# Kernel optimization log

Hardware: AMD Instinct MI355X
Metric: run time of the kernel (lower is better)

## Reference

```python
import jax, jax.numpy as jnp
import numpy as np

# Int8 fixed-point (power-of-two scale) quant params, mirroring Brevitas
# Int8ActPerTensorFixedPoint / Uint8ActPerTensorFixedPoint with fixed learned scales.
QMAX, QMIN, UQMAX = 127.0, -128.0, 255.0
IO_SCALE = 2.0 ** -4    # io_quant (int8) range ~ [-8, 7.94]
ACC_SCALE = 2.0 ** -3   # gate_acc_quant (int8) range ~ [-16, 15.875]
SIG_SCALE = 2.0 ** -8   # sigmoid_quant (uint8) range [0, ~0.996]
TANH_SCALE = 2.0 ** -7  # tanh_quant (int8) range ~ [-1, 0.992]


def ste_round(x):
    return x + jax.lax.stop_gradient(jnp.round(x) - x)


def qd(x, scale, qmin, qmax):
    # quantize-dequantize with straight-through rounding
    return scale * jnp.clip(ste_round(x / scale), qmin, qmax)


def quant_weight(w):
    # Int8WeightPerTensorFixedPoint: power-of-two per-tensor scale from max-abs stats
    maxabs = jax.lax.stop_gradient(jnp.max(jnp.abs(w)))
    scale = jax.lax.stop_gradient(2.0 ** jnp.ceil(jnp.log2(maxabs / QMAX)))
    return qd(w, scale, QMIN, QMAX)


def setup_inputs() -> dict:
    key = jax.random.key(0)
    ks = jax.random.split(key, 8)
    B, S, V, E, H, O = 64, 512, 32000, 512, 512, 2
    return {
        "text": jax.random.randint(ks[0], (B, S), 0, V, dtype=jnp.int32),
        "text_lengths": jax.random.randint(ks[1], (B,), 1, S, dtype=jnp.int32),
        "emb_w": jax.random.normal(ks[2], (V, E), jnp.float32) * 0.05,
        "w_ih": jax.random.normal(ks[3], (4 * H, E), jnp.float32) * 0.05,
        "w_hh": jax.random.normal(ks[4], (4 * H, H), jnp.float32) * 0.05,
        "b_ih": jax.random.normal(ks[5], (4 * H,), jnp.float32) * 0.05,
        "b_hh": jax.random.normal(ks[6], (4 * H,), jnp.float32) * 0.05,
        "fc_w": jax.random.normal(ks[7], (O, H), jnp.float32) * 0.05,
    }


def reference(text, text_lengths, emb_w, w_ih, w_hh, b_ih, b_hh, fc_w):
    B = text.shape[0]
    H = w_hh.shape[1]

    # quantized embedding lookup + io quant on LSTM input
    x = quant_weight(emb_w)[text]               # [B,S,E]
    x = qd(x, IO_SCALE, QMIN, QMAX)

    wih_q = quant_weight(w_ih)
    whh_q = quant_weight(w_hh)

    # precompute input contribution to gates: [B,S,4H]
    xg = jnp.einsum("bse,ge->bsg", x, wih_q) + b_ih + b_hh

    def step(carry, xg_t):
        h, c = carry
        gates = qd(xg_t + h @ whh_q.T, ACC_SCALE, QMIN, QMAX)  # gate_acc quant
        i, f, g, o = jnp.split(gates, 4, axis=-1)
        i = qd(jax.nn.sigmoid(i), SIG_SCALE, 0.0, UQMAX)
        f = qd(jax.nn.sigmoid(f), SIG_SCALE, 0.0, UQMAX)
        o = qd(jax.nn.sigmoid(o), SIG_SCALE, 0.0, UQMAX)
        g = qd(jnp.tanh(g), TANH_SCALE, QMIN, QMAX)
        c = f * c + i * g
        h = qd(o * qd(jnp.tanh(c), TANH_SCALE, QMIN, QMAX), IO_SCALE, QMIN, QMAX)
        return (h, c), h

    h0 = jnp.zeros((B, H), x.dtype)
    (hT, cT), _ = jax.lax.scan(step, (h0, h0), jnp.swapaxes(xg, 0, 1))

    hidden_state = hT[None]                     # [1,B,H] like torch LSTM
    return hidden_state @ quant_weight(fc_w).T  # [1,B,O]
```

## Files before the change

### kernel.cpp

```cpp
#include <hip/hip_runtime.h>
#include <math.h>

#define S_LEN  512
#define BATCH  64
#define E_DIM  512
#define H_DIM  512
#define G4     2048
#define VOCAB  32000
#define NWG    16

typedef int v4i __attribute__((ext_vector_type(4)));
typedef unsigned long long u64;

#define O_BAR   0
#define O_MAX   256
#define O_H8    512
#define O_FC8   131584
#define O_WIH8  132608
#define O_WHH8  (O_WIH8 + 1048576)
#define O_X8    (O_WHH8 + 1048576)

__device__ __forceinline__ float clampf(float x, float lo, float hi) {
    return fminf(fmaxf(x, lo), hi);
}

__device__ __forceinline__ int scale_exp(float maxabs) {
    double t = (double)maxabs / 127.0;
    int e; double f = frexp(t, &e);
    return (f == 0.5) ? (e - 1) : e;
}

__device__ __forceinline__ float xla_tanhf(float x) {
    if (fabsf(x) < 0.0004f) return x;
    float xc = fminf(fmaxf(x, -7.90531110763549805f), 7.90531110763549805f);
    float x2 = __fmul_rn(xc, xc);
    float p = fmaf(x2, -2.76076847742355e-16f, 2.00018790482477e-13f);
    p = fmaf(x2, p, -8.60467152213735e-11f);
    p = fmaf(x2, p, 5.12229709037114e-08f);
    p = fmaf(x2, p, 1.48572235717979e-05f);
    p = fmaf(x2, p, 6.37261928875436e-04f);
    p = fmaf(x2, p, 4.89352455891786e-03f);
    p = __fmul_rn(xc, p);
    float q = fmaf(x2, 1.19825839466702e-06f, 1.18534705686654e-04f);
    q = fmaf(x2, q, 2.26843463243900e-03f);
    q = fmaf(x2, q, 4.89352518554385e-03f);
    return __fdiv_rn(p, q);
}

__global__ void k_maxabs(const float* __restrict__ x, int n, unsigned* __restrict__ out) {
    unsigned m = 0;
    for (int i = blockIdx.x * blockDim.x + threadIdx.x; i < n; i += gridDim.x * blockDim.x)
        m = max(m, __float_as_uint(fabsf(x[i])));
    #pragma unroll
    for (int o = 32; o > 0; o >>= 1) {
        unsigned other = (unsigned)__shfl_down((int)m, o, 64);
        m = max(m, other);
    }
    __shared__ unsigned sm[4];
    if ((threadIdx.x & 63) == 0) sm[threadIdx.x >> 6] = m;
    __syncthreads();
    if (threadIdx.x == 0) {
        unsigned r = sm[0];
        for (int w = 1; w < (int)(blockDim.x >> 6); w++) r = max(r, sm[w]);
        atomicMax(out, r);
    }
}

__global__ void k_quantw(const float* __restrict__ w, int n, const unsigned* __restrict__ mx,
                         signed char* __restrict__ q) {
    float inv = ldexpf(1.0f, -scale_exp(__uint_as_float(*mx)));
    for (int i = blockIdx.x * blockDim.x + threadIdx.x; i < n; i += gridDim.x * blockDim.x) {
        float v = clampf(rintf(w[i] * inv), -128.0f, 127.0f);
        q[i] = (signed char)(int)v;
    }
}

__global__ void k_embed(const float* __restrict__ emb, const int* __restrict__ text,
                        const unsigned* __restrict__ mx, signed char* __restrict__ x8) {
    int row = blockIdx.x;
    int b = row >> 9, s = row & 511;
    int tok = text[row];
    int ke = scale_exp(__uint_as_float(*mx));
    float inv = ldexpf(1.0f, -ke);
    float sc2 = ldexpf(1.0f, ke + 4);
    const float4* src = (const float4*)(emb + (size_t)tok * E_DIM);
    char4* dst = (char4*)(x8 + (size_t)(s * BATCH + b) * E_DIM);
    float4 v = src[threadIdx.x];
    char4 c;
    float q;
    q = clampf(rintf(v.x * inv), -128.f, 127.f); c.x = (signed char)(int)clampf(rintf(q * sc2), -128.f, 127.f);
    q = clampf(rintf(v.y * inv), -128.f, 127.f); c.y = (signed char)(int)clampf(rintf(q * sc2), -128.f, 127.f);
    q = clampf(rintf(v.z * inv), -128.f, 127.f); c.z = (signed char)(int)clampf(rintf(q * sc2), -128.f, 127.f);
    q = clampf(rintf(v.w * inv), -128.f, 127.f); c.w = (signed char)(int)clampf(rintf(q * sc2), -128.f, 127.f);
    dst[threadIdx.x] = c;
}

#define MKFRAG(a, b) ((v4i){(a)[0], (a)[1], (b)[0], (b)[1]})

__global__ __launch_bounds__(256, 1) void k_lstm(
    const signed char* __restrict__ wih8, const signed char* __restrict__ whh8,
    const signed char* __restrict__ x8, const float* __restrict__ b_ih,
    const float* __restrict__ b_hh, const unsigned* __restrict__ mx,
    signed char* __restrict__ h8) {
    __shared__ __attribute__((aligned(16))) signed char wih_lds[128 * 528];
    __shared__ __attribute__((aligned(16))) signed char hstage[BATCH * 32];
    __shared__ float lut_sig[256];
    __shared__ float lut_tnh[256];

    const int g = blockIdx.x;
    const int tid = threadIdx.x;
    const int wv = tid >> 6, lane = tid & 63, l15 = lane & 15, qd4 = lane >> 4;
    const float sih = ldexpf(1.0f, scale_exp(__uint_as_float(mx[1])) - 4);
    const float shh = ldexpf(1.0f, scale_exp(__uint_as_float(mx[2])) - 4);

    if (tid < 256) {
        float v = (float)(tid - 128) * 0.125f;
        float sg = __fadd_rn(0.5f, __fmul_rn(0.5f, xla_tanhf(__fmul_rn(0.5f, v))));
        float sc = clampf(rintf(__fmul_rn(sg, 256.0f)), 0.0f, 255.0f);
        lut_sig[tid] = sc * 0.00390625f;
        float th = xla_tanhf(v);
        float tc = clampf(rintf(__fmul_rn(th, 128.0f)), -128.0f, 127.0f);
        lut_tnh[tid] = tc * 0.0078125f;
    }

    for (int it = 0; it < 16; it++) {
        int idx = it * 256 + tid;
        int r = idx >> 5, cc = (idx & 31) * 16;
        int grow = (r >> 5) * 512 + g * 32 + (r & 31);
        *(v4i*)(wih_lds + r * 528 + cc) = *(const v4i*)(wih8 + (size_t)grow * 512 + cc);
    }

    v4i whf[8][8];
    #pragma unroll
    for (int nt = 0; nt < 8; nt++) {
        int nl = nt * 16 + l15;
        size_t grow = (size_t)((nl >> 5) * 512 + g * 32 + (nl & 31)) * 512;
        #pragma unroll
        for (int k = 0; k < 8; k++)
            whf[nt][k] = *(const v4i*)(whh8 + grow + k * 64 + qd4 * 16);
    }
    __syncthreads();

    float bi[8], bh[8];
    #pragma unroll
    for (int nt = 0; nt < 8; nt++) {
        int nl = nt * 16 + l15;
        int col = (nl >> 5) * 512 + g * 32 + (nl & 31);
        bi[nt] = b_ih[col];
        bh[nt] = b_hh[col];
    }

    float cst[2][4];
    #pragma unroll
    for (int jh = 0; jh < 2; jh++)
        #pragma unroll
        for (int r = 0; r < 4; r++) cst[jh][r] = 0.0f;

    v4i xacc[8];
    {
        v4i xfr[8];
        const signed char* xrow = x8 + (size_t)(wv * 16 + l15) * 512 + qd4 * 16;
        #pragma unroll
        for (int k = 0; k < 8; k++) xfr[k] = *(const v4i*)(xrow + k * 64);
        #pragma unroll
        for (int nt = 0; nt < 8; nt++) {
            v4i a = (v4i){0, 0, 0, 0};
            #pragma unroll
            for (int k = 0; k < 8; k++) {
                v4i bf = *(const v4i*)(wih_lds + (nt * 16 + l15) * 528 + k * 64 + qd4 * 16);
                a = __builtin_amdgcn_mfma_i32_16x16x64_i8(xfr[k], bf, a, 0, 0, 0);
            }
            xacc[nt] = a;
        }
    }

    const int row = wv * 16 + l15;
    const int pb = tid >> 2, psub = tid & 3;
    const u64 paddr_base = (u64)(h8) + (u64)(pb * 64 + g * 4 + psub) * 16;
    const u64 caddr_base = (u64)(h8) + (u64)(row * 64 + qd4 * 2) * 16;

    for (int t = 0; t < S_LEN; t++) {
        u64 ha = caddr_base + (u64)(t & 1) * 65536;
        int tg = t;
        v4i u0,u1,u2,u3,u4,u5,u6,u7,u8,u9,u10,u11,u12,u13,u14,u15;
        for (;;) {
            asm volatile(
                "global_load_dwordx4 %0,  %16, off sc0 sc1\n\t"
                "global_load_dwordx4 %1,  %16, off offset:16 sc0 sc1\n\t"
                "global_load_dwordx4 %2,  %16, off offset:128 sc0 sc1\n\t"
                "global_load_dwordx4 %3,  %16, off offset:144 sc0 sc1\n\t"
                "global_load_dwordx4 %4,  %16, off offset:256 sc0 sc1\n\t"
                "global_load_dwordx4 %5,  %16, off offset:272 sc0 sc1\n\t"
                "global_load_dwordx4 %6,  %16, off offset:384 sc0 sc1\n\t"
                "global_load_dwordx4 %7,  %16, off offset:400 sc0 sc1\n\t"
                "global_load_dwordx4 %8,  %16, off offset:512 sc0 sc1\n\t"
                "global_load_dwordx4 %9,  %16, off offset:528 sc0 sc1\n\t"
                "global_load_dwordx4 %10, %16, off offset:640 sc0 sc1\n\t"
                "global_load_dwordx4 %11, %16, off offset:656 sc0 sc1\n\t"
                "global_load_dwordx4 %12, %16, off offset:768 sc0 sc1\n\t"
                "global_load_dwordx4 %13, %16, off offset:784 sc0 sc1\n\t"
                "global_load_dwordx4 %14, %16, off offset:896 sc0 sc1\n\t"
                "global_load_dwordx4 %15, %16, off offset:912 sc0 sc1\n\t"
                "s_waitcnt vmcnt(0)"
                : "=&v"(u0), "=&v"(u1), "=&v"(u2), "=&v"(u3),
                  "=&v"(u4), "=&v"(u5), "=&v"(u6), "=&v"(u7),
                  "=&v"(u8), "=&v"(u9), "=&v"(u10), "=&v"(u11),
                  "=&v"(u12), "=&v"(u13), "=&v"(u14), "=&v"(u15)
                : "v"(ha)
                : "memory");
            bool ok = (u0[2] == tg) & (u1[2] == tg) & (u2[2] == tg) & (u3[2] == tg)
                    & (u4[2] == tg) & (u5[2] == tg) & (u6[2] == tg) & (u7[2] == tg)
                    & (u8[2] == tg) & (u9[2] == tg) & (u10[2] == tg) & (u11[2] == tg)
                    & (u12[2] == tg) & (u13[2] == tg) & (u14[2] == tg) & (u15[2] == tg);
            if (ok) break;
            __builtin_amdgcn_s_sleep(1);
        }
        v4i afr[8];
        afr[0] = MKFRAG(u0, u1);   afr[1] = MKFRAG(u2, u3);
        afr[2] = MKFRAG(u4, u5);   afr[3] = MKFRAG(u6, u7);
        afr[4] = MKFRAG(u8, u9);   afr[5] = MKFRAG(u10, u11);
        afr[6] = MKFRAG(u12, u13); afr[7] = MKFRAG(u14, u15);

        float pre[8][4];
        #pragma unroll
        for (int nt = 0; nt < 8; nt++) {
            v4i hacc = (v4i){0, 0, 0, 0};
            #pragma unroll
            for (int k = 0; k < 8; k++)
                hacc = __builtin_amdgcn_mfma_i32_16x16x64_i8(afr[k], whf[nt][k], hacc, 0, 0, 0);
            #pragma unroll
            for (int r = 0; r < 4; r++)
                pre[nt][r] = __fadd_rn(
                    __fadd_rn(__fadd_rn(__fmul_rn((float)xacc[nt][r], sih), bi[nt]), bh[nt]),
                    __fmul_rn((float)hacc[r], shh));
        }

        #pragma unroll
        for (int jh = 0; jh < 2; jh++)
            #pragma unroll
            for (int r = 0; r < 4; r++) {
                int ii = (int)clampf(rintf(__fmul_rn(pre[0 + jh][r], 8.0f)), -128.f, 127.f) + 128;
                int fi = (int)clampf(rintf(__fmul_rn(pre[2 + jh][r], 8.0f)), -128.f, 127.f) + 128;
                int gi = (int)clampf(rintf(__fmul_rn(pre[4 + jh][r], 8.0f)), -128.f, 127.f) + 128;
                int oi = (int)clampf(rintf(__fmul_rn(pre[6 + jh][r], 8.0f)), -128.f, 127.f) + 128;
                float iq = lut_sig[ii], fq = lut_sig[fi], oq = lut_sig[oi];
                float gq = lut_tnh[gi];
                float c = __fadd_rn(__fmul_rn(fq, cst[jh][r]), __fmul_rn(iq, gq));
                cst[jh][r] = c;
                float tc32 = xla_tanhf(c);
                float tq = clampf(rintf(__fmul_rn(tc32, 128.0f)), -128.f, 127.f) * 0.0078125f;
                float hv = __fmul_rn(oq, tq);
                int hc = (int)clampf(rintf(__fmul_rn(hv, 16.0f)), -128.f, 127.f);
                int b = wv * 16 + qd4 * 4 + r;
                hstage[b * 32 + jh * 16 + l15] = (signed char)hc;
            }

        {
            u64 codes = *(const u64*)(hstage + tid * 8);
            v4i sval = (v4i){(int)(codes & 0xffffffffu), (int)(codes >> 32), t + 1, 0};
            u64 pa = paddr_base + (u64)((t + 1) & 1) * 65536;
            asm volatile("global_store_dwordx4 %0, %1, off sc0 sc1\n\t"
                         "s_waitcnt vmcnt(0)"
                         :: "v"(pa), "v"(sval) : "memory");
        }

        if (t + 1 < S_LEN) {
            v4i xfr[8];
            const signed char* xrow = x8 + (size_t)((t + 1) * BATCH + wv * 16 + l15) * 512 + qd4 * 16;
            #pragma unroll
            for (int k = 0; k < 8; k++) xfr[k] = *(const v4i*)(xrow + k * 64);
            #pragma unroll
            for (int nt = 0; nt < 8; nt++) {
                v4i a = (v4i){0, 0, 0, 0};
                #pragma unroll
                for (int k = 0; k < 8; k++) {
                    v4i bf = *(const v4i*)(wih_lds + (nt * 16 + l15) * 528 + k * 64 + qd4 * 16);
                    a = __builtin_amdgcn_mfma_i32_16x16x64_i8(xfr[k], bf, a, 0, 0, 0);
                }
                xacc[nt] = a;
            }
        }
    }
}

__global__ void k_fc(const signed char* __restrict__ h8, const signed char* __restrict__ fc8,
                     const unsigned* __restrict__ mx_fc, float* __restrict__ out) {
    int tid = threadIdx.x;
    int b = tid >> 1, o = tid & 1;
    const signed char* hp = h8 + b * 1024;
    const char4* wp = (const char4*)(fc8 + o * 512);
    int s = 0;
    for (int i = 0; i < 64; i++) {
        u64 hv = __hip_atomic_load((const u64*)(hp + i * 16), __ATOMIC_RELAXED, __HIP_MEMORY_SCOPE_AGENT);
        char4 w0 = wp[i * 2], w1 = wp[i * 2 + 1];
        signed char hb[8];
        *(u64*)hb = hv;
        s += hb[0] * w0.x + hb[1] * w0.y + hb[2] * w0.z + hb[3] * w0.w
           + hb[4] * w1.x + hb[5] * w1.y + hb[6] * w1.z + hb[7] * w1.w;
    }
    float sc = ldexpf(1.0f, scale_exp(__uint_as_float(*mx_fc)) - 4);
    out[b * 2 + o] = (float)s * sc;
}

extern "C" void kernel_launch(void* const* d_in, const int* in_sizes, int n_in,
                              void* d_out, int out_size, void* d_ws, size_t ws_size,
                              hipStream_t stream) {
    (void)in_sizes; (void)n_in; (void)out_size; (void)ws_size;
    const int*   text = (const int*)d_in[0];
    const float* emb  = (const float*)d_in[2];
    const float* w_ih = (const float*)d_in[3];
    const float* w_hh = (const float*)d_in[4];
    const float* b_ih = (const float*)d_in[5];
    const float* b_hh = (const float*)d_in[6];
    const float* fc_w = (const float*)d_in[7];

    char* ws = (char*)d_ws;
    unsigned*    mx   = (unsigned*)(ws + O_MAX);
    signed char* h8   = (signed char*)(ws + O_H8);
    signed char* fc8  = (signed char*)(ws + O_FC8);
    signed char* wih8 = (signed char*)(ws + O_WIH8);
    signed char* whh8 = (signed char*)(ws + O_WHH8);
    signed char* x8   = (signed char*)(ws + O_X8);

    hipMemsetAsync(d_ws, 0, O_H8 + 2 * 65536, stream);

    k_maxabs<<<2048, 256, 0, stream>>>(emb, VOCAB * E_DIM, mx + 0);
    k_maxabs<<<256, 256, 0, stream>>>(w_ih, G4 * E_DIM, mx + 1);
    k_maxabs<<<256, 256, 0, stream>>>(w_hh, G4 * H_DIM, mx + 2);
    k_maxabs<<<1, 256, 0, stream>>>(fc_w, 2 * H_DIM, mx + 3);

    k_quantw<<<512, 256, 0, stream>>>(w_ih, G4 * E_DIM, mx + 1, wih8);
    k_quantw<<<512, 256, 0, stream>>>(w_hh, G4 * H_DIM, mx + 2, whh8);
    k_quantw<<<2, 256, 0, stream>>>(fc_w, 2 * H_DIM, mx + 3, fc8);

    k_embed<<<BATCH * S_LEN, 128, 0, stream>>>(emb, text, mx + 0, x8);

    k_lstm<<<NWG, 256, 0, stream>>>(wih8, whh8, x8, b_ih, b_hh, mx, h8);

    k_fc<<<1, 128, 0, stream>>>(h8, fc8, mx + 3, (float*)d_out);
}
```

Measured before the change: 3.187 ms.

## Replace tag-in-data polling with per-wave flag array for LSTM step sync

Cross-workgroup hidden-state exchange used to poll 16 vector loads per lane until every chunk carried the current step tag. Now each wave spins on one small per-(wave, workgroup) flag word using system-scope atomic reads. After the flag check passes, it fetches the hidden-state codes once with 64-bit atomic loads, and writers publish the flag after their data store. This cuts polling traffic on the h buffer, at the cost of a second serialized round trip (flag, then data) on each recurrent step. Ordering depends on relaxed atomics plus the writer's waitcnt.

```diff
diff --git a/kernel.cpp b/kernel.cpp
--- a/kernel.cpp
+++ b/kernel.cpp
@@ -13,10 +13,11 @@
 typedef unsigned long long u64;
 
 #define O_BAR   0
-#define O_MAX   256
-#define O_H8    512
-#define O_FC8   131584
-#define O_WIH8  132608
+#define O_FLG   256
+#define O_MAX   768
+#define O_H8    1024
+#define O_FC8   (O_H8 + 131072)
+#define O_WIH8  (O_FC8 + 1024)
 #define O_WHH8  (O_WIH8 + 1048576)
 #define O_X8    (O_WHH8 + 1048576)
 
@@ -95,13 +96,11 @@
     dst[threadIdx.x] = c;
 }
 
-#define MKFRAG(a, b) ((v4i){(a)[0], (a)[1], (b)[0], (b)[1]})
-
 __global__ __launch_bounds__(256, 1) void k_lstm(
     const signed char* __restrict__ wih8, const signed char* __restrict__ whh8,
     const signed char* __restrict__ x8, const float* __restrict__ b_ih,
     const float* __restrict__ b_hh, const unsigned* __restrict__ mx,
-    signed char* __restrict__ h8) {
+    signed char* __restrict__ h8, unsigned* __restrict__ flg) {
     __shared__ __attribute__((aligned(16))) signed char wih_lds[128 * 528];
     __shared__ __attribute__((aligned(16))) signed char hstage[BATCH * 32];
     __shared__ float lut_sig[256];
@@ -178,48 +177,34 @@
     const int pb = tid >> 2, psub = tid & 3;
     const u64 paddr_base = (u64)(h8) + (u64)(pb * 64 + g * 4 + psub) * 16;
     const u64 caddr_base = (u64)(h8) + (u64)(row * 64 + qd4 * 2) * 16;
+    unsigned* const frd = flg + wv * 16 + l15;
+    unsigned* const fwr = flg + wv * 16 + g;
 
     for (int t = 0; t < S_LEN; t++) {
+        {
+            unsigned* fa = frd + (t & 1) * 64;
+            for (;;) {
+                unsigned fv = __hip_atomic_fetch_add(fa, 0u, __ATOMIC_RELAXED,
+                                                     __HIP_MEMORY_SCOPE_SYSTEM);
+                if (__all(fv == (unsigned)t)) break;
+                __builtin_amdgcn_s_sleep(1);
+            }
+        }
+
         u64 ha = caddr_base + (u64)(t & 1) * 65536;
-        int tg = t;
-        v4i u0,u1,u2,u3,u4,u5,u6,u7,u8,u9,u10,u11,u12,u13,u14,u15;
-        for (;;) {
-            asm volatile(
-                "global_load_dwordx4 %0,  %16, off sc0 sc1\n\t"
-                "global_load_dwordx4 %1,  %16, off offset:16 sc0 sc1\n\t"
-                "global_load_dwordx4 %2,  %16, off offset:128 sc0 sc1\n\t"
-                "global_load_dwordx4 %3,  %16, off offset:144 sc0 sc1\n\t"
-                "global_load_dwordx4 %4,  %16, off offset:256 sc0 sc1\n\t"
-                "global_load_dwordx4 %5,  %16, off offset:272 sc0 sc1\n\t"
-                "global_load_dwordx4 %6,  %16, off offset:384 sc0 sc1\n\t"
-                "global_load_dwordx4 %7,  %16, off offset:400 sc0 sc1\n\t"
-                "global_load_dwordx4 %8,  %16, off offset:512 sc0 sc1\n\t"
-                "global_load_dwordx4 %9,  %16, off offset:528 sc0 sc1\n\t"
-                "global_load_dwordx4 %10, %16, off offset:640 sc0 sc1\n\t"
-                "global_load_dwordx4 %11, %16, off offset:656 sc0 sc1\n\t"
-                "global_load_dwordx4 %12, %16, off offset:768 sc0 sc1\n\t"
-                "global_load_dwordx4 %13, %16, off offset:784 sc0 sc1\n\t"
-                "global_load_dwordx4 %14, %16, off offset:896 sc0 sc1\n\t"
-                "global_load_dwordx4 %15, %16, off offset:912 sc0 sc1\n\t"
-                "s_waitcnt vmcnt(0)"
-                : "=&v"(u0), "=&v"(u1), "=&v"(u2), "=&v"(u3),
-                  "=&v"(u4), "=&v"(u5), "=&v"(u6), "=&v"(u7),
-                  "=&v"(u8), "=&v"(u9), "=&v"(u10), "=&v"(u11),
-                  "=&v"(u12), "=&v"(u13), "=&v"(u14), "=&v"(u15)
-                : "v"(ha)
-                : "memory");
-            bool ok = (u0[2] == tg) & (u1[2] == tg) & (u2[2] == tg) & (u3[2] == tg)
-                    & (u4[2] == tg) & (u5[2] == tg) & (u6[2] == tg) & (u7[2] == tg)
-                    & (u8[2] == tg) & (u9[2] == tg) & (u10[2] == tg) & (u11[2] == tg)
-                    & (u12[2] == tg) & (u13[2] == tg) & (u14[2] == tg) & (u15[2] == tg);
-            if (ok) break;
-            __builtin_amdgcn_s_sleep(1);
+        u64 c[16];
+        #pragma unroll
+        for (int k = 0; k < 8; k++) {
+            c[2 * k] = __hip_atomic_fetch_add((u64*)(ha + (u64)k * 128), 0ull,
+                                              __ATOMIC_RELAXED, __HIP_MEMORY_SCOPE_SYSTEM);
+            c[2 * k + 1] = __hip_atomic_fetch_add((u64*)(ha + (u64)k * 128 + 16), 0ull,
+                                                  __ATOMIC_RELAXED, __HIP_MEMORY_SCOPE_SYSTEM);
         }
         v4i afr[8];
-        afr[0] = MKFRAG(u0, u1);   afr[1] = MKFRAG(u2, u3);
-        afr[2] = MKFRAG(u4, u5);   afr[3] = MKFRAG(u6, u7);
-        afr[4] = MKFRAG(u8, u9);   afr[5] = MKFRAG(u10, u11);
-        afr[6] = MKFRAG(u12, u13); afr[7] = MKFRAG(u14, u15);
+        #pragma unroll
+        for (int i = 0; i < 8; i++)
+            afr[i] = (v4i){(int)(c[2 * i] & 0xffffffffu), (int)(c[2 * i] >> 32),
+                           (int)(c[2 * i + 1] & 0xffffffffu), (int)(c[2 * i + 1] >> 32)};
 
         float pre[8][4];
         #pragma unroll
@@ -245,9 +230,9 @@
                 int oi = (int)clampf(rintf(__fmul_rn(pre[6 + jh][r], 8.0f)), -128.f, 127.f) + 128;
                 float iq = lut_sig[ii], fq = lut_sig[fi], oq = lut_sig[oi];
                 float gq = lut_tnh[gi];
-                float c = __fadd_rn(__fmul_rn(fq, cst[jh][r]), __fmul_rn(iq, gq));
-                cst[jh][r] = c;
-                float tc32 = xla_tanhf(c);
+                float c2 = __fadd_rn(__fmul_rn(fq, cst[jh][r]), __fmul_rn(iq, gq));
+                cst[jh][r] = c2;
+                float tc32 = xla_tanhf(c2);
                 float tq = clampf(rintf(__fmul_rn(tc32, 128.0f)), -128.f, 127.f) * 0.0078125f;
                 float hv = __fmul_rn(oq, tq);
                 int hc = (int)clampf(rintf(__fmul_rn(hv, 16.0f)), -128.f, 127.f);
@@ -262,6 +247,9 @@
             asm volatile("global_store_dwordx4 %0, %1, off sc0 sc1\n\t"
                          "s_waitcnt vmcnt(0)"
                          :: "v"(pa), "v"(sval) : "memory");
+            if (lane == 0)
+                __hip_atomic_exchange(fwr + ((t + 1) & 1) * 64, (unsigned)(t + 1),
+                                      __ATOMIC_RELAXED, __HIP_MEMORY_SCOPE_SYSTEM);
         }
 
         if (t + 1 < S_LEN) {
@@ -315,6 +303,7 @@
     const float* fc_w = (const float*)d_in[7];
 
     char* ws = (char*)d_ws;
+    unsigned*    flg  = (unsigned*)(ws + O_FLG);
     unsigned*    mx   = (unsigned*)(ws + O_MAX);
     signed char* h8   = (signed char*)(ws + O_H8);
     signed char* fc8  = (signed char*)(ws + O_FC8);
@@ -335,7 +324,7 @@
 
     k_embed<<<BATCH * S_LEN, 128, 0, stream>>>(emb, text, mx + 0, x8);
 
-    k_lstm<<<NWG, 256, 0, stream>>>(wih8, whh8, x8, b_ih, b_hh, mx, h8);
+    k_lstm<<<NWG, 256, 0, stream>>>(wih8, whh8, x8, b_ih, b_hh, mx, h8, flg);
 
     k_fc<<<1, 128, 0, stream>>>(h8, fc8, mx + 3, (float*)d_out);
 }
```

After: 3.332 ms. +4.6%, slower.
